# Optimization experiments

Hardware: AMD Instinct MI355X
Metric: run time of the kernel (lower is better)

Reference implementation:

```python
import jax, jax.numpy as jnp
import numpy as np
from jax import lax

NUM_HOP = 2      # opt.num_hop
POOL_HOP = 1     # Encoder(..., num_hop=1) in gnn_pools
K_POOL = 1024    # int(pooling_ratio * num_patches) = 0.5 * 2048
TH = 0.0         # opt.nonzero_th
T = 0.07         # NCE temperature
NEG_FILL = -10.0


def l2norm(x):
    # Normalize(power=2): x / (sum(x^2, dim=1, keepdim)^(1/2))
    return x / jnp.sqrt(jnp.sum(x * x, axis=1, keepdims=True))


def tagconv(A, h, W, b, k):
    # DGL TAGConv: concat_{i=0..k} (D^-1/2 A D^-1/2)^i h, then linear
    deg = jnp.sum(A, axis=1)
    dinv = lax.rsqrt(jnp.maximum(deg, 1e-12))
    An = A * dinv[:, None] * dinv[None, :]   # [N,N] normalized adjacency
    feats = [h]
    for _ in range(k):
        h = An @ h
        feats.append(h)
    return jnp.concatenate(feats, axis=1) @ W + b


def nce_pair(f_t, f_s):
    # calc_gnn NCE: positives = diag(f_t . f_s); negatives = full gram with diag masked to -10
    n = f_t.shape[0]
    eye = jnp.eye(n, dtype=bool)
    pos = jnp.sum(f_t * f_s, axis=1, keepdims=True)          # [N,1]
    neg_s = jnp.where(eye, NEG_FILL, f_t @ f_s.T)            # [N,N]
    neg_t = jnp.where(eye, NEG_FILL, f_s @ f_t.T)
    out_s = jnp.concatenate([pos, neg_s], axis=1) / T
    out_t = jnp.concatenate([pos, neg_t], axis=1) / T
    # CrossEntropy with label 0 == -log_softmax(out)[:, 0], mean over rows
    loss_s = -jnp.mean(jax.nn.log_softmax(out_s, axis=1)[:, 0])
    loss_t = -jnp.mean(jax.nn.log_softmax(out_t, axis=1)[:, 0])
    return loss_s + loss_t


def setup_inputs() -> dict:
    key = jax.random.key(0)
    ks = jax.random.split(key, 8)
    N, C, D = 2048, 512, 128
    g = 0.02  # init_gain ('normal' init)
    return {
        "fs": jax.random.normal(ks[0], (N, C), jnp.float32),
        "ft": jax.random.normal(ks[1], (N, C), jnp.float32),
        "W_embed": g * jax.random.normal(ks[2], (C, D), jnp.float32),
        "b_embed": jnp.zeros((D,), jnp.float32),
        "W_gnn": g * jax.random.normal(ks[3], ((NUM_HOP + 1) * D, D), jnp.float32),
        "b_gnn": jnp.zeros((D,), jnp.float32),
        "W_pool": g * jax.random.normal(ks[4], (D, 1), jnp.float32),
        "b_pool": jnp.zeros((1,), jnp.float32),
        "W_gnnp": g * jax.random.normal(ks[5], ((POOL_HOP + 1) * D, D), jnp.float32),
        "b_gnnp": jnp.zeros((D,), jnp.float32),
    }


def reference(fs, ft, W_embed, b_embed, W_gnn, b_gnn, W_pool, b_pool, W_gnnp, b_gnnp):
    # Embed: linear + l2 norm
    f_es = l2norm(fs @ W_embed + b_embed)   # student [N, nc]
    f_et = l2norm(ft @ W_embed + b_embed)   # teacher [N, nc]

    # nonzero_graph on detached teacher features; same adjacency reused for student
    ft_d = lax.stop_gradient(f_et)
    n = f_et.shape[0]
    eye = jnp.eye(n, dtype=bool)
    A = (ft_d @ ft_d.T > TH).astype(f_et.dtype)
    A = jnp.where(eye, 1.0, A)  # dgl.add_self_loop

    # TAGConv encoder + l2norm; teacher branch detached
    f_gt = lax.stop_gradient(l2norm(tagconv(A, f_et, W_gnn, b_gnn, NUM_HOP)))
    f_gs = l2norm(tagconv(A, f_es, W_gnn, b_gnn, NUM_HOP))
    loss_g = nce_pair(f_gt, f_gs)

    # Pool / top_k_graph
    scores = jax.nn.sigmoid((f_gt @ W_pool + b_pool)[:, 0])   # [N]
    vals, idx = lax.top_k(scores, K_POOL)
    new_ht = f_gt[idx] * vals[:, None]
    new_hs = f_gs[idx] * vals[:, None]
    un = (A > 0).astype(A.dtype)
    un2 = ((un @ un) > 0).astype(A.dtype)        # 2-hop boolean adjacency
    sub = un2[idx][:, idx]                       # [k,k]
    deg = jnp.sum(sub, axis=1)
    g_pool = sub / deg[None, :]                  # replicates torch broadcast in norm_g(g/degrees)

    # pooled-stage Encoder (TAGConv k=1) on the pooled graph structure (with self loops)
    k = K_POOL
    eye_k = jnp.eye(k, dtype=bool)
    Ap = (g_pool > 0).astype(A.dtype)
    Ap = jnp.where(eye_k, 1.0, Ap)
    f_pt = lax.stop_gradient(l2norm(tagconv(Ap, new_ht, W_gnnp, b_gnnp, POOL_HOP)))
    f_ps = l2norm(tagconv(Ap, new_hs, W_gnnp, b_gnnp, POOL_HOP))
    loss_pool = nce_pair(f_pt, f_ps)

    return loss_g + loss_pool
```

## Files before the change

kernel.cpp:

```cpp
#include <hip/hip_runtime.h>


#define TINV (1.0f / 0.07f)

using short8 = __attribute__((ext_vector_type(8))) short;
using f32x4  = __attribute__((ext_vector_type(4))) float;

__device__ __forceinline__ unsigned short f2bf(float f) {
    unsigned u = __float_as_uint(f);
    u += 0x7fff + ((u >> 16) & 1);
    return (unsigned short)(u >> 16);
}

template<bool BT>
__device__ __forceinline__ void mm_tile(const float* __restrict__ A, int lda,
                                        const float* __restrict__ B, int ldb,
                                        int i0, int j0, int k0, int k1,
                                        float (&acc)[4][4],
                                        float (&As)[16][68], float (&Bs)[16][68])
{
    const int tid = threadIdx.x;
    const int tx = tid & 15;
    const int ty = tid >> 4;
    const int lr = tid >> 2;
    const int lc = (tid & 3) * 4;
    for (int k = k0; k < k1; k += 16) {
        float4 av = *(const float4*)(A + (size_t)(i0 + lr) * lda + (k + lc));
        As[lc + 0][lr] = av.x; As[lc + 1][lr] = av.y;
        As[lc + 2][lr] = av.z; As[lc + 3][lr] = av.w;
        if (BT) {
            float4 bv = *(const float4*)(B + (size_t)(j0 + lr) * ldb + (k + lc));
            Bs[lc + 0][lr] = bv.x; Bs[lc + 1][lr] = bv.y;
            Bs[lc + 2][lr] = bv.z; Bs[lc + 3][lr] = bv.w;
        } else {
            const int n = tid & 63;
            const int kb = tid >> 6;
#pragma unroll
            for (int it = 0; it < 4; ++it)
                Bs[kb * 4 + it][n] = B[(size_t)(k + kb * 4 + it) * ldb + (j0 + n)];
        }
        __syncthreads();
#pragma unroll
        for (int kk = 0; kk < 16; ++kk) {
            float a[4], b[4];
#pragma unroll
            for (int u = 0; u < 4; ++u) a[u] = As[kk][ty * 4 + u];
#pragma unroll
            for (int v = 0; v < 4; ++v) b[v] = Bs[kk][tx * 4 + v];
#pragma unroll
            for (int u = 0; u < 4; ++u)
#pragma unroll
                for (int v = 0; v < 4; ++v)
                    acc[u][v] = fmaf(a[u], b[v], acc[u][v]);
        }
        __syncthreads();
    }
}

__launch_bounds__(256)
__global__ void k_setup_embed(const float* __restrict__ fs, const float* __restrict__ ft,
                              const float* __restrict__ W, float* __restrict__ part,
                              size_t zstr, int* __restrict__ zwords, int zcount,
                              float* __restrict__ out,
                              const float* __restrict__ Wg, const float* __restrict__ Wp,
                              unsigned short* __restrict__ Wtall)
{
    __shared__ float As[16][68];
    __shared__ float Bs[16][68];
    const int b = blockIdx.x;
    const int tid = threadIdx.x;
    if (b < 512) {
        const int z = b & 3;
        const int by = (b >> 2) & 63;
        const int bx = b >> 8;
        const float* A = (by < 32) ? ft : fs;
        const int i0 = (by & 31) * 64;
        const int j0 = bx * 64;
        float acc[4][4] = {};
        mm_tile<false>(A, 512, W, 128, i0, j0, z * 128, z * 128 + 128, acc, As, Bs);
        const int tx = tid & 15, ty = tid >> 4;
        float* dst = part + (size_t)z * zstr;
#pragma unroll
        for (int u = 0; u < 4; ++u) {
            const size_t ri = (size_t)(by * 64 + ty * 4 + u) * 128 + j0 + tx * 4;
#pragma unroll
            for (int v = 0; v < 4; ++v) dst[ri + v] = acc[u][v];
        }
    } else if (b < 561) {
        const int i = (b - 512) * 256 + tid;
        if (i < zcount) zwords[i] = 0;
        if (b == 512 && tid == 0) out[0] = 0.0f;
    } else {
        const int e0 = (b - 561) * 2048 + tid;
#pragma unroll
        for (int it = 0; it < 8; ++it) {
            const int e = e0 + it * 256;
            const int c = e >> 14;
            const int rem = e & 16383;
            const int n = rem >> 7, k = rem & 127;
            const float* src = (c < 3) ? (Wg + (size_t)c * 16384)
                                       : (Wp + (size_t)(c - 3) * 16384);
            Wtall[e] = f2bf(src[(size_t)k * 128 + n]);
        }
    }
}

__launch_bounds__(256)
__global__ void k_gram_fused(const float* __restrict__ f_e,
                             unsigned short* __restrict__ A01,
                             unsigned long long* __restrict__ bits,
                             int* __restrict__ deg)
{
    __shared__ float As[16][68];
    __shared__ float Bs[16][68];
    __shared__ unsigned char nib[64][16];
    __shared__ unsigned char nibT[64][16];
    __shared__ unsigned long long chk[64];
    __shared__ unsigned long long chkT[64];
    const int b = blockIdx.x;
    int by = (int)((sqrtf(8.0f * b + 1.0f) - 1.0f) * 0.5f);
    while ((by + 1) * (by + 2) / 2 <= b) ++by;
    while (by * (by + 1) / 2 > b) --by;
    const int bx = b - by * (by + 1) / 2;
    const int i0 = by * 64, j0 = bx * 64;
    float acc[4][4] = {};
    mm_tile<true>(f_e, 128, f_e, 128, i0, j0, 0, 128, acc, As, Bs);
    const int tid = threadIdx.x;
    const int tx = tid & 15, ty = tid >> 4;
    unsigned pb = 0;
#pragma unroll
    for (int u = 0; u < 4; ++u)
#pragma unroll
        for (int v = 0; v < 4; ++v) {
            bool pred = (acc[u][v] > 0.0f) || (i0 + ty * 4 + u == j0 + tx * 4 + v);
            pb |= (unsigned)pred << (u * 4 + v);
        }
#pragma unroll
    for (int u = 0; u < 4; ++u) nib[ty * 4 + u][tx] = (pb >> (4 * u)) & 15;
#pragma unroll
    for (int v = 0; v < 4; ++v) {
        unsigned nt = 0;
#pragma unroll
        for (int u = 0; u < 4; ++u) nt |= ((pb >> (u * 4 + v)) & 1u) << u;
        nibT[tx * 4 + v][ty] = nt;
    }
    __syncthreads();
    if (tid < 64) {
        unsigned long long c = 0;
#pragma unroll
        for (int t = 0; t < 16; ++t) c |= (unsigned long long)nib[tid][t] << (4 * t);
        chk[tid] = c;
        bits[(size_t)(i0 + tid) * 32 + (j0 >> 6)] = c;
        atomicAdd(&deg[i0 + tid], __popcll(c));
    } else if (tid < 128 && bx != by) {
        const int r = tid - 64;
        unsigned long long c = 0;
#pragma unroll
        for (int t = 0; t < 16; ++t) c |= (unsigned long long)nibT[r][t] << (4 * t);
        chkT[r] = c;
        bits[(size_t)(j0 + r) * 32 + (i0 >> 6)] = c;
        atomicAdd(&deg[j0 + r], __popcll(c));
    }
    __syncthreads();
#pragma unroll
    for (int it = 0; it < 16; ++it) {
        const int row = it * 4 + (tid >> 6);
        const int col = tid & 63;
        A01[(size_t)(i0 + row) * 2048 + j0 + col] =
            ((chk[row] >> col) & 1) ? (unsigned short)0x3F80 : (unsigned short)0;
        if (bx != by)
            A01[(size_t)(j0 + row) * 2048 + i0 + col] =
                ((chkT[row] >> col) & 1) ? (unsigned short)0x3F80 : (unsigned short)0;
    }
}

__launch_bounds__(256)
__global__ void mm_bf16(const unsigned short* __restrict__ A, int lda, size_t aZ,
                        const unsigned short* __restrict__ B, int ldb, size_t bZ,
                        float* __restrict__ C, int ldc, size_t cZ,
                        int Kc, int kZ)
{
    __shared__ unsigned short As[64][40];
    __shared__ unsigned short Bs[128][40];
    const int tid = threadIdx.x;
    const int bz = blockIdx.z;
    const int i0 = blockIdx.y * 64;
    const int j0 = blockIdx.x * 128;
    const int k0 = bz * kZ;
    const unsigned short* Ab = A + (size_t)bz * aZ;
    const unsigned short* Bb = B + (size_t)bz * bZ;
    float* Cb = C + (size_t)bz * cZ;
    const int w = tid >> 6;
    const int lane = tid & 63;
    const int m = lane & 15;
    const int q = lane >> 4;
    f32x4 acc[8];
#pragma unroll
    for (int t = 0; t < 8; ++t)
#pragma unroll
        for (int r = 0; r < 4; ++r) acc[t][r] = 0.0f;

    const int ar = tid >> 2;
    const int ac = (tid & 3) * 8;
    for (int ks = 0; ks < Kc; ks += 32) {
        const int k = k0 + ks;
        *(ulonglong2*)&As[ar][ac] =
            *(const ulonglong2*)(Ab + (size_t)(i0 + ar) * lda + k + ac);
        *(ulonglong2*)&Bs[ar][ac] =
            *(const ulonglong2*)(Bb + (size_t)(j0 + ar) * ldb + k + ac);
        *(ulonglong2*)&Bs[ar + 64][ac] =
            *(const ulonglong2*)(Bb + (size_t)(j0 + ar + 64) * ldb + k + ac);
        __syncthreads();
        short8 a = *(const short8*)&As[w * 16 + m][q * 8];
#pragma unroll
        for (int nt = 0; nt < 8; ++nt) {
            short8 b = *(const short8*)&Bs[nt * 16 + m][q * 8];
            acc[nt] = __builtin_amdgcn_mfma_f32_16x16x32_bf16(a, b, acc[nt], 0, 0, 0);
        }
        __syncthreads();
    }
#pragma unroll
    for (int nt = 0; nt < 8; ++nt) {
        const int col = j0 + nt * 16 + m;
#pragma unroll
        for (int r = 0; r < 4; ++r) {
            const int row = i0 + w * 16 + q * 4 + r;
            Cb[(size_t)row * ldc + col] = acc[nt][r];
        }
    }
}

__global__ void reduce_hop(const float* __restrict__ part, int nz, size_t zstr,
                           int M, const float* __restrict__ dinv,
                           unsigned short* __restrict__ hb,
                           unsigned short* __restrict__ xt)
{
    __shared__ float T[32][33];
    const int tid = threadIdx.x;
    const int iloc = tid >> 3, nq = (tid & 7) * 4;
    const int n = blockIdx.x * 32 + nq;
    const int i = blockIdx.y * 32 + iloc;
    float4 s = *(const float4*)(part + (size_t)i * 256 + n);
    for (int z = 1; z < nz; ++z) {
        float4 t = *(const float4*)(part + (size_t)z * zstr + (size_t)i * 256 + n);
        s.x += t.x; s.y += t.y; s.z += t.z; s.w += t.w;
    }
    const float d = dinv[i];
    unsigned short o[4] = { f2bf(s.x * d), f2bf(s.y * d), f2bf(s.z * d), f2bf(s.w * d) };
    const int hrow = (n >= 128 ? M : 0) + i;
    *(ulonglong1*)(hb + (size_t)hrow * 128 + (n & 127)) = *(ulonglong1*)o;
    if (xt) {
        const float d2 = d * d;
        T[nq + 0][iloc] = s.x * d2; T[nq + 1][iloc] = s.y * d2;
        T[nq + 2][iloc] = s.z * d2; T[nq + 3][iloc] = s.w * d2;
        __syncthreads();
        const int nloc = tid >> 3, ic = (tid & 7) * 4;
        unsigned short o2[4];
#pragma unroll
        for (int c = 0; c < 4; ++c) o2[c] = f2bf(T[nloc][ic + c]);
        *(ulonglong1*)(xt + (size_t)(blockIdx.x * 32 + nloc) * M + blockIdx.y * 32 + ic) =
            *(ulonglong1*)o2;
    }
}

__global__ void combine_norm(const float* __restrict__ part, int nz, size_t zstr,
                             const float* __restrict__ bias,
                             float* __restrict__ f32out,
                             unsigned short* __restrict__ bf16out,
                             const float* __restrict__ Wp, const float* __restrict__ bp,
                             float* __restrict__ scores)
{
    const int row = blockIdx.x;
    const int tid = threadIdx.x;
    float v = bias[tid];
    for (int z = 0; z < nz; ++z) v += part[(size_t)z * zstr + (size_t)row * 128 + tid];
    __shared__ float red[128];
    red[tid] = v * v;
    __syncthreads();
    for (int s = 64; s > 0; s >>= 1) {
        if (tid < s) red[tid] += red[tid + s];
        __syncthreads();
    }
    const float o = v * (1.0f / sqrtf(red[0]));
    if (f32out)  f32out[(size_t)row * 128 + tid] = o;
    if (bf16out) bf16out[(size_t)row * 128 + tid] = f2bf(o);
    if (scores && row < 2048) {
        __syncthreads();
        red[tid] = o * Wp[tid];
        __syncthreads();
        for (int s = 64; s > 0; s >>= 1) {
            if (tid < s) red[tid] += red[tid + s];
            __syncthreads();
        }
        if (tid == 0) scores[row] = 1.0f / (1.0f + expf(-(red[0] + bp[0])));
    }
}

__global__ void make_xt(const float* __restrict__ f_e, const int* __restrict__ deg,
                        unsigned short* __restrict__ xt, float* __restrict__ dinv)
{
    __shared__ float T[32][33];
    const int b = blockIdx.x;
    const int bx = b & 7, by = b >> 3;
    const int tid = threadIdx.x;
    const int iloc = tid >> 3, nq = (tid & 7) * 4;
    const int n0 = bx * 32;
    const int i = by * 32 + iloc;
    const int srow = (n0 >= 128 ? 2048 : 0) + i;
    float4 f = *(const float4*)(f_e + (size_t)srow * 128 + ((n0 + nq) & 127));
    const float d = 1.0f / sqrtf((float)deg[i]);
    if (bx == 0 && (tid & 7) == 0) dinv[i] = d;
    T[nq + 0][iloc] = f.x * d; T[nq + 1][iloc] = f.y * d;
    T[nq + 2][iloc] = f.z * d; T[nq + 3][iloc] = f.w * d;
    __syncthreads();
    const int nloc = tid >> 3, ic = (tid & 7) * 4;
    unsigned short o[4];
#pragma unroll
    for (int c = 0; c < 4; ++c) o[c] = f2bf(T[nloc][ic + c]);
    *(ulonglong1*)(xt + (size_t)(n0 + nloc) * 2048 + by * 32 + ic) = *(ulonglong1*)o;
}

__launch_bounds__(256)
__global__ void k_nce_topk(const unsigned short* __restrict__ A,
                           const unsigned short* __restrict__ B,
                           float* __restrict__ rowsum, float* __restrict__ colsum,
                           float* __restrict__ pos, int gramBlocks, int bw,
                           const float* __restrict__ scores,
                           float* __restrict__ vals, int* __restrict__ idx)
{
    __shared__ unsigned short As[64][40];
    __shared__ unsigned short Bs[128][40];
    __shared__ float colbuf[4][128];
    __shared__ unsigned sv[2048];
    __shared__ int hist[256];
    __shared__ int shp, shr, sh_base, sh_out, wsum[5];
    const int tid = threadIdx.x;
    const int b = blockIdx.x;
    if (b < gramBlocks) {
        const int bx = b % bw, by = b / bw;
        const int i0 = by * 64;
        const int j0 = bx * 128;
        const int w = tid >> 6;
        const int lane = tid & 63;
        const int m = lane & 15;
        const int q = lane >> 4;
        f32x4 acc[8];
#pragma unroll
        for (int t = 0; t < 8; ++t)
#pragma unroll
            for (int r = 0; r < 4; ++r) acc[t][r] = 0.0f;
        const int ar = tid >> 2;
        const int ac = (tid & 3) * 8;
        for (int k = 0; k < 128; k += 32) {
            *(ulonglong2*)&As[ar][ac] =
                *(const ulonglong2*)(A + (size_t)(i0 + ar) * 128 + k + ac);
            *(ulonglong2*)&Bs[ar][ac] =
                *(const ulonglong2*)(B + (size_t)(j0 + ar) * 128 + k + ac);
            *(ulonglong2*)&Bs[ar + 64][ac] =
                *(const ulonglong2*)(B + (size_t)(j0 + ar + 64) * 128 + k + ac);
            __syncthreads();
            short8 a = *(const short8*)&As[w * 16 + m][q * 8];
#pragma unroll
            for (int nt = 0; nt < 8; ++nt) {
                short8 bb = *(const short8*)&Bs[nt * 16 + m][q * 8];
                acc[nt] = __builtin_amdgcn_mfma_f32_16x16x32_bf16(a, bb, acc[nt], 0, 0, 0);
            }
            __syncthreads();
        }
        float rpart[4] = {0.0f, 0.0f, 0.0f, 0.0f};
        float cpart[8];
#pragma unroll
        for (int nt = 0; nt < 8; ++nt) {
            const int col = j0 + nt * 16 + m;
            float cs = 0.0f;
#pragma unroll
            for (int r = 0; r < 4; ++r) {
                const int row = i0 + w * 16 + q * 4 + r;
                float g = acc[nt][r];
                float e = __expf(g * TINV);
                if (row == col) { pos[row] = g; e = 0.0f; }
                rpart[r] += e;
                cs += e;
            }
            cpart[nt] = cs;
        }
#pragma unroll
        for (int r = 0; r < 4; ++r) {
            float v = rpart[r];
            v += __shfl_xor(v, 1); v += __shfl_xor(v, 2);
            v += __shfl_xor(v, 4); v += __shfl_xor(v, 8);
            if (m == 0) atomicAdd(&rowsum[i0 + w * 16 + q * 4 + r], v);
        }
#pragma unroll
        for (int nt = 0; nt < 8; ++nt) {
            float v = cpart[nt];
            v += __shfl_xor(v, 16); v += __shfl_xor(v, 32);
            if (q == 0) colbuf[w][nt * 16 + m] = v;
        }
        __syncthreads();
        if (tid < 128) {
            float v = colbuf[0][tid] + colbuf[1][tid] + colbuf[2][tid] + colbuf[3][tid];
            atomicAdd(&colsum[j0 + tid], v);
        }
    } else {
        for (int e = tid; e < 2048; e += 256) sv[e] = __float_as_uint(scores[e]);
        if (tid == 0) { shp = 0; shr = 1024; sh_base = 0; sh_out = 0; }
        __syncthreads();
        for (int byte = 3; byte >= 0; --byte) {
            hist[tid] = 0;
            __syncthreads();
            const unsigned pref = (unsigned)shp;
            const unsigned pmask = (byte == 3) ? 0u : (0xFFFFFFFFu << ((byte + 1) * 8));
            for (int e = tid; e < 2048; e += 256) {
                unsigned u = sv[e];
                if ((u & pmask) == (pref & pmask))
                    atomicAdd(&hist[(u >> (byte * 8)) & 255], 1);
            }
            __syncthreads();
            if (tid == 0) {
                int rem = shr, bs = 255;
                for (; bs > 0; --bs) {
                    if (hist[bs] >= rem) break;
                    rem -= hist[bs];
                }
                shp = (int)(pref | ((unsigned)bs << (byte * 8)));
                shr = rem;
            }
            __syncthreads();
        }
        const unsigned t = (unsigned)shp;
        const int remain = shr;
        const int lane = tid & 63, wave = tid >> 6;
        for (int pass = 0; pass < 8; ++pass) {
            const int e = pass * 256 + tid;
            const unsigned u = sv[e];
            const bool eq = (u == t);
            unsigned long long mk = __ballot(eq);
            int wpre = __popcll(mk & ((1ull << lane) - 1ull));
            if (lane == 0) wsum[wave] = __popcll(mk);
            __syncthreads();
            if (tid == 0) {
                int a = sh_base;
                for (int ww = 0; ww < 4; ++ww) { int c = wsum[ww]; wsum[ww] = a; a += c; }
                sh_base = a;
            }
            __syncthreads();
            const int rank = eq ? (wsum[wave] + wpre) : 0x7fffffff;
            if ((u > t) || (eq && rank < remain)) {
                int slot = atomicAdd(&sh_out, 1);
                idx[slot] = e;
                vals[slot] = __uint_as_float(u);
            }
            __syncthreads();
        }
    }
}

__global__ void k_final_ap(const float* __restrict__ rs, const float* __restrict__ cs,
                           const float* __restrict__ pos, float* __restrict__ out,
                           const unsigned long long* __restrict__ bits,
                           const int* __restrict__ idx,
                           unsigned short* __restrict__ Ap, int* __restrict__ degp)
{
    __shared__ unsigned long long pb[16][33];
    __shared__ unsigned long long qb[16][33];
    __shared__ float red[256];
    const int b = blockIdx.x;
    const int tid = threadIdx.x;
    if (b < 4096) {
        const int tp = (b >> 6) * 16;
        const int tq = (b & 63) * 16;
        for (int t = tid; t < 512; t += 256) {
            int r = t >> 5, w = t & 31;
            pb[r][w] = bits[(size_t)idx[tp + r] * 32 + w];
            qb[r][w] = bits[(size_t)idx[tq + r] * 32 + w];
        }
        __syncthreads();
        const int pi = tid >> 4, qi = tid & 15;
        unsigned long long acc = 0;
#pragma unroll
        for (int w = 0; w < 32; ++w) acc |= (pb[pi][w] & qb[qi][w]);
        Ap[(size_t)(tp + pi) * 1024 + tq + qi] =
            acc ? (unsigned short)0x3F80 : (unsigned short)0;
        int v = acc ? 1 : 0;
        v += __shfl_xor(v, 1); v += __shfl_xor(v, 2);
        v += __shfl_xor(v, 4); v += __shfl_xor(v, 8);
        if (qi == 0) atomicAdd(&degp[tp + pi], v);
    } else {
        const int i = (b - 4096) * 256 + tid;
        float p = pos[i] * TINV;
        float ep = __expf(p);
        float t = (logf(rs[i] + ep) - p) + (logf(cs[i] + ep) - p);
        red[tid] = t;
        __syncthreads();
        for (int s = 128; s > 0; s >>= 1) {
            if (tid < s) red[tid] += red[tid + s];
            __syncthreads();
        }
        if (tid == 0) atomicAdd(out, red[0] * (1.0f / 2048.0f));
    }
}

__global__ void nce_final(const float* __restrict__ rs, const float* __restrict__ cs,
                          const float* __restrict__ pos, float invN,
                          float* __restrict__ out)
{
    const int i = blockIdx.x * 256 + threadIdx.x;
    float p = pos[i] * TINV;
    float ep = __expf(p);
    float t = (logf(rs[i] + ep) - p) + (logf(cs[i] + ep) - p);
    __shared__ float red[256];
    red[threadIdx.x] = t;
    __syncthreads();
    for (int s = 128; s > 0; s >>= 1) {
        if (threadIdx.x < s) red[threadIdx.x] += red[threadIdx.x + s];
        __syncthreads();
    }
    if (threadIdx.x == 0) atomicAdd(out, red[0] * invN);
}

__global__ void gather_xt(const float* __restrict__ f_g, const int* __restrict__ idx,
                          const float* __restrict__ vals, const int* __restrict__ degp,
                          unsigned short* __restrict__ new_hb,
                          unsigned short* __restrict__ xtp, float* __restrict__ dinvp)
{
    __shared__ float T[32][33];
    const int b = blockIdx.x;
    const int bx = b & 7, by = b >> 3;
    const int tid = threadIdx.x;
    const int ploc = tid >> 3, nq = (tid & 7) * 4;
    const int n0 = bx * 32;
    const int p = by * 32 + ploc;
    const int s = idx[p];
    const float v = vals[p];
    const float dp = 1.0f / sqrtf((float)degp[p]);
    if (bx == 0 && (tid & 7) == 0) dinvp[p] = dp;
    const int srow = (n0 >= 128 ? 2048 : 0) + s;
    float4 f = *(const float4*)(f_g + (size_t)srow * 128 + ((n0 + nq) & 127));
    f.x *= v; f.y *= v; f.z *= v; f.w *= v;
    unsigned short o[4] = { f2bf(f.x), f2bf(f.y), f2bf(f.z), f2bf(f.w) };
    const int hrow = (n0 >= 128 ? 1024 : 0) + p;
    *(ulonglong1*)(new_hb + (size_t)hrow * 128 + ((n0 + nq) & 127)) = *(ulonglong1*)o;
    T[nq + 0][ploc] = f.x * dp; T[nq + 1][ploc] = f.y * dp;
    T[nq + 2][ploc] = f.z * dp; T[nq + 3][ploc] = f.w * dp;
    __syncthreads();
    const int nloc = tid >> 3, pc = (tid & 7) * 4;
    unsigned short o2[4];
#pragma unroll
    for (int c = 0; c < 4; ++c) o2[c] = f2bf(T[nloc][pc + c]);
    *(ulonglong1*)(xtp + (size_t)(n0 + nloc) * 1024 + by * 32 + pc) = *(ulonglong1*)o2;
}

extern "C" void kernel_launch(void* const* d_in, const int* in_sizes, int n_in,
                              void* d_out, int out_size, void* d_ws, size_t ws_size,
                              hipStream_t stream)
{
    (void)in_sizes; (void)n_in; (void)out_size; (void)ws_size;
    const float* fs      = (const float*)d_in[0];
    const float* ft      = (const float*)d_in[1];
    const float* W_embed = (const float*)d_in[2];
    const float* b_embed = (const float*)d_in[3];
    const float* W_gnn   = (const float*)d_in[4];
    const float* b_gnn   = (const float*)d_in[5];
    const float* W_pool  = (const float*)d_in[6];
    const float* b_pool  = (const float*)d_in[7];
    const float* W_gnnp  = (const float*)d_in[8];
    const float* b_gnnp  = (const float*)d_in[9];
    float* out = (float*)d_out;

    float* ws = (float*)d_ws;
    size_t o = 0;
    auto alloc = [&](size_t n) { float* p = ws + o; o += (n + 3) & ~3ull; return p; };
    float* bigB   = alloc(2048ull * 2048);
    float* f_e    = alloc(4096 * 128);
    float* f_g    = alloc(4096 * 128);
    unsigned short* A01  = (unsigned short*)alloc(2048ull * 2048 / 2);
    unsigned short* febT = (unsigned short*)alloc(3ull * 4096 * 128 / 2);
    unsigned short* Xt1  = (unsigned short*)alloc(256ull * 2048 / 2);
    unsigned short* Xt2  = (unsigned short*)alloc(256ull * 2048 / 2);
    unsigned short* f_gb = (unsigned short*)alloc(4096ull * 128 / 2);
    unsigned short* Wtall= (unsigned short*)alloc(5ull * 16384 / 2);
    unsigned short* Ap01 = (unsigned short*)alloc(1024ull * 1024 / 2);
    unsigned short* nhb  = (unsigned short*)alloc(2ull * 2048 * 128 / 2);
    unsigned short* Xtp  = (unsigned short*)alloc(256ull * 1024 / 2);
    unsigned short* f_pb = (unsigned short*)alloc(2048ull * 128 / 2);
    float* dinv   = alloc(2048);
    float* scores = alloc(2048);
    float* vals   = alloc(1024);
    int*   idxb   = (int*)alloc(1024);
    float* dinvp  = alloc(1024);
    unsigned long long* bits = (unsigned long long*)alloc(2048 * 32 * 2);
    float* nceb = alloc(9216);
    int*   deg  = (int*)alloc(2048);
    int*   degp = (int*)alloc(1024);
    const int kZeroCount = 9216 + 2048 + 1024;

    const size_t FSTR = 4096ull * 128;
    const size_t PSTR = 1024ull * 256;
    unsigned short* feb = febT;
    unsigned short* h1b = febT + FSTR;
    unsigned short* h2b = febT + 2 * FSTR;
    unsigned short* tmpb = nhb + 2048ull * 128;
    unsigned short* Wt  = Wtall;
    unsigned short* WtP = Wtall + 3ull * 16384;
    float* rs  = nceb;
    float* csu = nceb + 2048;
    float* pos = nceb + 4096;
    float* rsp  = nceb + 6144;
    float* csp  = nceb + 7168;
    float* posp = nceb + 8192;

    k_setup_embed<<<601, 256, 0, stream>>>(fs, ft, W_embed, bigB, FSTR,
                                           (int*)nceb, kZeroCount, out, W_gnn, W_gnnp, Wtall);
    combine_norm<<<4096, 128, 0, stream>>>(bigB, 4, FSTR, b_embed, f_e, feb,
                                           nullptr, nullptr, nullptr);
    k_gram_fused<<<528, 256, 0, stream>>>(f_e, A01, bits, deg);
    make_xt<<<512, 256, 0, stream>>>(f_e, deg, Xt1, dinv);
    mm_bf16<<<dim3(2, 32, 8), 256, 0, stream>>>(A01, 2048, 0, Xt1, 2048, 0,
                                                bigB, 256, FSTR, 256, 256);
    reduce_hop<<<dim3(8, 64), 256, 0, stream>>>(bigB, 8, FSTR, 2048, dinv, h1b, Xt2);
    mm_bf16<<<dim3(2, 32, 8), 256, 0, stream>>>(A01, 2048, 0, Xt2, 2048, 0,
                                                bigB, 256, FSTR, 256, 256);
    reduce_hop<<<dim3(8, 64), 256, 0, stream>>>(bigB, 8, FSTR, 2048, dinv, h2b, nullptr);
    mm_bf16<<<dim3(1, 64, 3), 256, 0, stream>>>(feb, 128, FSTR, Wt, 128, 16384,
                                                bigB, 128, FSTR, 128, 0);
    combine_norm<<<4096, 128, 0, stream>>>(bigB, 3, FSTR, b_gnn, f_g, f_gb,
                                           W_pool, b_pool, scores);
    k_nce_topk<<<513, 256, 0, stream>>>(f_gb, f_gb + 2048 * 128, rs, csu, pos,
                                        512, 16, scores, vals, idxb);
    k_final_ap<<<4104, 256, 0, stream>>>(rs, csu, pos, out, bits, idxb, Ap01, degp);
    gather_xt<<<256, 256, 0, stream>>>(f_g, idxb, vals, degp, nhb, Xtp, dinvp);
    mm_bf16<<<dim3(2, 16, 8), 256, 0, stream>>>(Ap01, 1024, 0, Xtp, 1024, 0,
                                                bigB, 256, PSTR, 128, 128);
    reduce_hop<<<dim3(8, 32), 256, 0, stream>>>(bigB, 8, PSTR, 1024, dinvp, tmpb, nullptr);
    mm_bf16<<<dim3(1, 32, 2), 256, 0, stream>>>(nhb, 128, 2048ull * 128, WtP, 128, 16384,
                                                bigB, 128, PSTR, 128, 0);
    combine_norm<<<2048, 128, 0, stream>>>(bigB, 2, PSTR, b_gnnp, nullptr, f_pb,
                                           nullptr, nullptr, nullptr);
    k_nce_topk<<<128, 256, 0, stream>>>(f_pb, f_pb + 1024 * 128, rsp, csp, posp,
                                        128, 8, nullptr, nullptr, nullptr);
    nce_final<<<4, 256, 0, stream>>>(rsp, csp, posp, 1.0f / 1024.0f, out);
}
```

Before: 227.3 us.

## Feed hop matmuls from packed adjacency bits and store bf16 split-K partials

Drops the dense bf16 0/1 adjacency matrices (2048x2048 and 1024x1024). A new matmul kernel expands the packed bitmask into bf16 tiles in shared memory on the fly. The pooled adjacency is now written as bits with atomicOr, and its zeroing moves into the setup kernel. Split-K partial results are stored as bf16 instead of fp32, which halves reduction traffic but adds rounding error before the sum.

```diff
diff --git a/kernel.cpp b/kernel.cpp
--- a/kernel.cpp
+++ b/kernel.cpp
@@ -10,6 +10,9 @@
     unsigned u = __float_as_uint(f);
     u += 0x7fff + ((u >> 16) & 1);
     return (unsigned short)(u >> 16);
+}
+__device__ __forceinline__ float bf2f(unsigned u16) {
+    return __uint_as_float(u16 << 16);
 }
 
 template<bool BT>
@@ -86,12 +89,12 @@
 #pragma unroll
             for (int v = 0; v < 4; ++v) dst[ri + v] = acc[u][v];
         }
-    } else if (b < 561) {
+    } else if (b < 688) {
         const int i = (b - 512) * 256 + tid;
         if (i < zcount) zwords[i] = 0;
         if (b == 512 && tid == 0) out[0] = 0.0f;
     } else {
-        const int e0 = (b - 561) * 2048 + tid;
+        const int e0 = (b - 688) * 2048 + tid;
 #pragma unroll
         for (int it = 0; it < 8; ++it) {
             const int e = e0 + it * 256;
@@ -107,7 +110,6 @@
 
 __launch_bounds__(256)
 __global__ void k_gram_fused(const float* __restrict__ f_e,
-                             unsigned short* __restrict__ A01,
                              unsigned long long* __restrict__ bits,
                              int* __restrict__ deg)
 {
@@ -115,8 +117,6 @@
     __shared__ float Bs[16][68];
     __shared__ unsigned char nib[64][16];
     __shared__ unsigned char nibT[64][16];
-    __shared__ unsigned long long chk[64];
-    __shared__ unsigned long long chkT[64];
     const int b = blockIdx.x;
     int by = (int)((sqrtf(8.0f * b + 1.0f) - 1.0f) * 0.5f);
     while ((by + 1) * (by + 2) / 2 <= b) ++by;
@@ -149,7 +149,6 @@
         unsigned long long c = 0;
 #pragma unroll
         for (int t = 0; t < 16; ++t) c |= (unsigned long long)nib[tid][t] << (4 * t);
-        chk[tid] = c;
         bits[(size_t)(i0 + tid) * 32 + (j0 >> 6)] = c;
         atomicAdd(&deg[i0 + tid], __popcll(c));
     } else if (tid < 128 && bx != by) {
@@ -157,20 +156,69 @@
         unsigned long long c = 0;
 #pragma unroll
         for (int t = 0; t < 16; ++t) c |= (unsigned long long)nibT[r][t] << (4 * t);
-        chkT[r] = c;
         bits[(size_t)(j0 + r) * 32 + (i0 >> 6)] = c;
         atomicAdd(&deg[j0 + r], __popcll(c));
     }
-    __syncthreads();
-#pragma unroll
-    for (int it = 0; it < 16; ++it) {
-        const int row = it * 4 + (tid >> 6);
-        const int col = tid & 63;
-        A01[(size_t)(i0 + row) * 2048 + j0 + col] =
-            ((chk[row] >> col) & 1) ? (unsigned short)0x3F80 : (unsigned short)0;
-        if (bx != by)
-            A01[(size_t)(j0 + row) * 2048 + i0 + col] =
-                ((chkT[row] >> col) & 1) ? (unsigned short)0x3F80 : (unsigned short)0;
+}
+
+__launch_bounds__(256)
+__global__ void mm_hopbits(const unsigned long long* __restrict__ bits, int wpr,
+                           const unsigned short* __restrict__ B, int ldb,
+                           unsigned short* __restrict__ C, size_t cZ,
+                           int Kc, int kZ)
+{
+    __shared__ unsigned short As[64][40];
+    __shared__ unsigned short Bs[128][40];
+    const int tid = threadIdx.x;
+    const int i0 = blockIdx.y * 64;
+    const int j0 = blockIdx.x * 128;
+    const int k0 = blockIdx.z * kZ;
+    unsigned short* Cb = C + (size_t)blockIdx.z * cZ;
+    const int w = tid >> 6;
+    const int lane = tid & 63;
+    const int m = lane & 15;
+    const int q = lane >> 4;
+    f32x4 acc[8];
+#pragma unroll
+    for (int t = 0; t < 8; ++t)
+#pragma unroll
+        for (int r = 0; r < 4; ++r) acc[t][r] = 0.0f;
+
+    const int ar = tid >> 2;
+    const int ac = (tid & 3) * 8;
+    for (int ks = 0; ks < Kc; ks += 32) {
+        const int k = k0 + ks;
+        const unsigned long long word = bits[(size_t)(i0 + ar) * wpr + ((k + ac) >> 6)];
+        const int sh = (k + ac) & 63;
+        unsigned long long lo = 0, hi = 0;
+#pragma unroll
+        for (int t = 0; t < 4; ++t) {
+            lo |= (((word >> (sh + t)) & 1ull) * 0x3F80ull) << (16 * t);
+            hi |= (((word >> (sh + 4 + t)) & 1ull) * 0x3F80ull) << (16 * t);
+        }
+        ulonglong2 pk; pk.x = lo; pk.y = hi;
+        *(ulonglong2*)&As[ar][ac] = pk;
+        *(ulonglong2*)&Bs[ar][ac] =
+            *(const ulonglong2*)(B + (size_t)(j0 + ar) * ldb + k + ac);
+        *(ulonglong2*)&Bs[ar + 64][ac] =
+            *(const ulonglong2*)(B + (size_t)(j0 + ar + 64) * ldb + k + ac);
+        __syncthreads();
+        short8 a = *(const short8*)&As[w * 16 + m][q * 8];
+#pragma unroll
+        for (int nt = 0; nt < 8; ++nt) {
+            short8 bb = *(const short8*)&Bs[nt * 16 + m][q * 8];
+            acc[nt] = __builtin_amdgcn_mfma_f32_16x16x32_bf16(a, bb, acc[nt], 0, 0, 0);
+        }
+        __syncthreads();
+    }
+#pragma unroll
+    for (int nt = 0; nt < 8; ++nt) {
+        const int col = j0 + nt * 16 + m;
+#pragma unroll
+        for (int r = 0; r < 4; ++r) {
+            const int row = i0 + w * 16 + q * 4 + r;
+            Cb[(size_t)row * 256 + col] = f2bf(acc[nt][r]);
+        }
     }
 }
 
@@ -230,7 +278,7 @@
     }
 }
 
-__global__ void reduce_hop(const float* __restrict__ part, int nz, size_t zstr,
+__global__ void reduce_hop(const unsigned short* __restrict__ part, int nz, size_t zstr,
                            int M, const float* __restrict__ dinv,
                            unsigned short* __restrict__ hb,
                            unsigned short* __restrict__ xt)
@@ -240,19 +288,23 @@
     const int iloc = tid >> 3, nq = (tid & 7) * 4;
     const int n = blockIdx.x * 32 + nq;
     const int i = blockIdx.y * 32 + iloc;
-    float4 s = *(const float4*)(part + (size_t)i * 256 + n);
-    for (int z = 1; z < nz; ++z) {
-        float4 t = *(const float4*)(part + (size_t)z * zstr + (size_t)i * 256 + n);
-        s.x += t.x; s.y += t.y; s.z += t.z; s.w += t.w;
+    float sx = 0.0f, sy = 0.0f, sz = 0.0f, sw = 0.0f;
+    for (int z = 0; z < nz; ++z) {
+        unsigned long long v = *(const unsigned long long*)
+            (part + (size_t)z * zstr + (size_t)i * 256 + n);
+        sx += bf2f((unsigned)(v & 0xFFFF));
+        sy += bf2f((unsigned)((v >> 16) & 0xFFFF));
+        sz += bf2f((unsigned)((v >> 32) & 0xFFFF));
+        sw += bf2f((unsigned)(v >> 48));
     }
     const float d = dinv[i];
-    unsigned short o[4] = { f2bf(s.x * d), f2bf(s.y * d), f2bf(s.z * d), f2bf(s.w * d) };
+    unsigned short o[4] = { f2bf(sx * d), f2bf(sy * d), f2bf(sz * d), f2bf(sw * d) };
     const int hrow = (n >= 128 ? M : 0) + i;
     *(ulonglong1*)(hb + (size_t)hrow * 128 + (n & 127)) = *(ulonglong1*)o;
     if (xt) {
         const float d2 = d * d;
-        T[nq + 0][iloc] = s.x * d2; T[nq + 1][iloc] = s.y * d2;
-        T[nq + 2][iloc] = s.z * d2; T[nq + 3][iloc] = s.w * d2;
+        T[nq + 0][iloc] = sx * d2; T[nq + 1][iloc] = sy * d2;
+        T[nq + 2][iloc] = sz * d2; T[nq + 3][iloc] = sw * d2;
         __syncthreads();
         const int nloc = tid >> 3, ic = (tid & 7) * 4;
         unsigned short o2[4];
@@ -460,7 +512,8 @@
                            const float* __restrict__ pos, float* __restrict__ out,
                            const unsigned long long* __restrict__ bits,
                            const int* __restrict__ idx,
-                           unsigned short* __restrict__ Ap, int* __restrict__ degp)
+                           unsigned long long* __restrict__ bitsP,
+                           int* __restrict__ degp)
 {
     __shared__ unsigned long long pb[16][33];
     __shared__ unsigned long long qb[16][33];
@@ -480,12 +533,16 @@
         unsigned long long acc = 0;
 #pragma unroll
         for (int w = 0; w < 32; ++w) acc |= (pb[pi][w] & qb[qi][w]);
-        Ap[(size_t)(tp + pi) * 1024 + tq + qi] =
-            acc ? (unsigned short)0x3F80 : (unsigned short)0;
+        const int lane = tid & 63;
+        unsigned long long mk = __ballot(acc != 0ull);
         int v = acc ? 1 : 0;
         v += __shfl_xor(v, 1); v += __shfl_xor(v, 2);
         v += __shfl_xor(v, 4); v += __shfl_xor(v, 8);
-        if (qi == 0) atomicAdd(&degp[tp + pi], v);
+        if (qi == 0) {
+            atomicAdd(&degp[tp + pi], v);
+            unsigned long long b16 = (mk >> ((lane >> 4) * 16)) & 0xFFFFull;
+            atomicOr(&bitsP[(size_t)(tp + pi) * 16 + (tq >> 6)], b16 << (tq & 63));
+        }
     } else {
         const int i = (b - 4096) * 256 + tid;
         float p = pos[i] * TINV;
@@ -574,13 +631,11 @@
     float* bigB   = alloc(2048ull * 2048);
     float* f_e    = alloc(4096 * 128);
     float* f_g    = alloc(4096 * 128);
-    unsigned short* A01  = (unsigned short*)alloc(2048ull * 2048 / 2);
     unsigned short* febT = (unsigned short*)alloc(3ull * 4096 * 128 / 2);
     unsigned short* Xt1  = (unsigned short*)alloc(256ull * 2048 / 2);
     unsigned short* Xt2  = (unsigned short*)alloc(256ull * 2048 / 2);
     unsigned short* f_gb = (unsigned short*)alloc(4096ull * 128 / 2);
     unsigned short* Wtall= (unsigned short*)alloc(5ull * 16384 / 2);
-    unsigned short* Ap01 = (unsigned short*)alloc(1024ull * 1024 / 2);
     unsigned short* nhb  = (unsigned short*)alloc(2ull * 2048 * 128 / 2);
     unsigned short* Xtp  = (unsigned short*)alloc(256ull * 1024 / 2);
     unsigned short* f_pb = (unsigned short*)alloc(2048ull * 128 / 2);
@@ -593,16 +648,20 @@
     float* nceb = alloc(9216);
     int*   deg  = (int*)alloc(2048);
     int*   degp = (int*)alloc(1024);
-    const int kZeroCount = 9216 + 2048 + 1024;
-
-    const size_t FSTR = 4096ull * 128;
-    const size_t PSTR = 1024ull * 256;
+    unsigned long long* bitsP = (unsigned long long*)alloc(32768);
+    const int kZeroCount = 9216 + 2048 + 1024 + 32768;
+
+    const size_t FSTR  = 4096ull * 128;
+    const size_t HSTR  = 2048ull * 256;
+    const size_t PSTRH = 1024ull * 256;
+    const size_t PSTR  = 1024ull * 256;
     unsigned short* feb = febT;
     unsigned short* h1b = febT + FSTR;
     unsigned short* h2b = febT + 2 * FSTR;
     unsigned short* tmpb = nhb + 2048ull * 128;
     unsigned short* Wt  = Wtall;
     unsigned short* WtP = Wtall + 3ull * 16384;
+    unsigned short* hpart = (unsigned short*)bigB;
     float* rs  = nceb;
     float* csu = nceb + 2048;
     float* pos = nceb + 4096;
@@ -610,29 +669,29 @@
     float* csp  = nceb + 7168;
     float* posp = nceb + 8192;
 
-    k_setup_embed<<<601, 256, 0, stream>>>(fs, ft, W_embed, bigB, FSTR,
+    k_setup_embed<<<728, 256, 0, stream>>>(fs, ft, W_embed, bigB, FSTR,
                                            (int*)nceb, kZeroCount, out, W_gnn, W_gnnp, Wtall);
     combine_norm<<<4096, 128, 0, stream>>>(bigB, 4, FSTR, b_embed, f_e, feb,
                                            nullptr, nullptr, nullptr);
-    k_gram_fused<<<528, 256, 0, stream>>>(f_e, A01, bits, deg);
+    k_gram_fused<<<528, 256, 0, stream>>>(f_e, bits, deg);
     make_xt<<<512, 256, 0, stream>>>(f_e, deg, Xt1, dinv);
-    mm_bf16<<<dim3(2, 32, 8), 256, 0, stream>>>(A01, 2048, 0, Xt1, 2048, 0,
-                                                bigB, 256, FSTR, 256, 256);
-    reduce_hop<<<dim3(8, 64), 256, 0, stream>>>(bigB, 8, FSTR, 2048, dinv, h1b, Xt2);
-    mm_bf16<<<dim3(2, 32, 8), 256, 0, stream>>>(A01, 2048, 0, Xt2, 2048, 0,
-                                                bigB, 256, FSTR, 256, 256);
-    reduce_hop<<<dim3(8, 64), 256, 0, stream>>>(bigB, 8, FSTR, 2048, dinv, h2b, nullptr);
+    mm_hopbits<<<dim3(2, 32, 8), 256, 0, stream>>>(bits, 32, Xt1, 2048,
+                                                   hpart, HSTR, 256, 256);
+    reduce_hop<<<dim3(8, 64), 256, 0, stream>>>(hpart, 8, HSTR, 2048, dinv, h1b, Xt2);
+    mm_hopbits<<<dim3(2, 32, 8), 256, 0, stream>>>(bits, 32, Xt2, 2048,
+                                                   hpart, HSTR, 256, 256);
+    reduce_hop<<<dim3(8, 64), 256, 0, stream>>>(hpart, 8, HSTR, 2048, dinv, h2b, nullptr);
     mm_bf16<<<dim3(1, 64, 3), 256, 0, stream>>>(feb, 128, FSTR, Wt, 128, 16384,
                                                 bigB, 128, FSTR, 128, 0);
     combine_norm<<<4096, 128, 0, stream>>>(bigB, 3, FSTR, b_gnn, f_g, f_gb,
                                            W_pool, b_pool, scores);
     k_nce_topk<<<513, 256, 0, stream>>>(f_gb, f_gb + 2048 * 128, rs, csu, pos,
                                         512, 16, scores, vals, idxb);
-    k_final_ap<<<4104, 256, 0, stream>>>(rs, csu, pos, out, bits, idxb, Ap01, degp);
+    k_final_ap<<<4104, 256, 0, stream>>>(rs, csu, pos, out, bits, idxb, bitsP, degp);
     gather_xt<<<256, 256, 0, stream>>>(f_g, idxb, vals, degp, nhb, Xtp, dinvp);
-    mm_bf16<<<dim3(2, 16, 8), 256, 0, stream>>>(Ap01, 1024, 0, Xtp, 1024, 0,
-                                                bigB, 256, PSTR, 128, 128);
-    reduce_hop<<<dim3(8, 32), 256, 0, stream>>>(bigB, 8, PSTR, 1024, dinvp, tmpb, nullptr);
+    mm_hopbits<<<dim3(2, 16, 8), 256, 0, stream>>>(bitsP, 16, Xtp, 1024,
+                                                   hpart, PSTRH, 128, 128);
+    reduce_hop<<<dim3(8, 32), 256, 0, stream>>>(hpart, 8, PSTRH, 1024, dinvp, tmpb, nullptr);
     mm_bf16<<<dim3(1, 32, 2), 256, 0, stream>>>(nhb, 128, 2048ull * 128, WtP, 128, 16384,
                                                 bigB, 128, PSTR, 128, 0);
     combine_norm<<<2048, 128, 0, stream>>>(bigB, 2, PSTR, b_gnnp, nullptr, f_pb,
```

New measurement: 233.3 us. 2.6% more time.
